# Performance work log

Measured on AMD Instinct MI355X. Metric: run time of the kernel, lower is better.

The kernel has to match this reference:

```python
import jax, jax.numpy as jnp
import numpy as np

SMOOTH = 1e-05


def setup_inputs() -> dict:
    key = jax.random.key(0)
    k1, k2 = jax.random.split(key)
    N, C, H, W = 8, 4, 1024, 1024
    inp = jax.random.normal(k1, (N, C, H, W), dtype=jnp.float32)
    target = jax.random.randint(k2, (N, H, W), 0, C, dtype=jnp.int32)
    weights = jnp.ones((C,), dtype=jnp.float32)
    return {"input": inp, "target": target, "weights": weights}


def reference(input, target, weights):
    # softmax over class dim
    p = jax.nn.softmax(input, axis=1)            # [N, C, H, W]
    C = input.shape[1]
    onehot = jax.nn.one_hot(target, C, axis=1, dtype=p.dtype)  # [N, C, H, W]
    # per-sample, per-class dice over flattened spatial dims
    inter = jnp.sum(p * onehot, axis=(2, 3))      # [N, C]
    denom = jnp.sum(p, axis=(2, 3)) + jnp.sum(onehot, axis=(2, 3))  # [N, C]
    dice = (2.0 * inter + SMOOTH) / (denom + SMOOTH)  # [N, C]
    per_class_loss = 1.0 - jnp.mean(dice, axis=0)     # [C]
    total = jnp.sum(per_class_loss * weights)
    return total
```

## Files before the change

### kernel.cpp

```cpp
#include <hip/hip_runtime.h>


#define HWPIX (1024 * 1024)
#define NCLS 4
#define NSMP 8
#define GX 256
#define TPB 256
#define NVEC (HWPIX / 4)
#define VSTRIDE (GX * TPB)
#define ITERS (NVEC / VSTRIDE)
static constexpr float SMOOTH = 1e-5f;

__global__ __launch_bounds__(TPB) void dice_partial(
    const float* __restrict__ inp,
    const int* __restrict__ tgt,
    float* __restrict__ part)
{
    const int n = blockIdx.y;
    const float4* __restrict__ in4 = (const float4*)(inp + (size_t)n * NCLS * HWPIX);
    const int4* __restrict__ tg4 = (const int4*)(tgt + (size_t)n * HWPIX);

    float psum0 = 0.f, psum1 = 0.f, psum2 = 0.f, psum3 = 0.f;
    float int0 = 0.f, int1 = 0.f, int2 = 0.f, int3 = 0.f;
    float cnt0 = 0.f, cnt1 = 0.f, cnt2 = 0.f, cnt3 = 0.f;

    const int base = blockIdx.x * TPB + threadIdx.x;

    #pragma unroll
    for (int s = 0; s < ITERS; ++s) {
        const int i = base + s * VSTRIDE;
        float4 x0 = in4[i];
        float4 x1 = in4[i + NVEC];
        float4 x2 = in4[i + 2 * NVEC];
        float4 x3 = in4[i + 3 * NVEC];
        int4 t4 = tg4[i];

        #pragma unroll
        for (int j = 0; j < 4; ++j) {
            float a = (j == 0) ? x0.x : (j == 1) ? x0.y : (j == 2) ? x0.z : x0.w;
            float b = (j == 0) ? x1.x : (j == 1) ? x1.y : (j == 2) ? x1.z : x1.w;
            float c = (j == 0) ? x2.x : (j == 1) ? x2.y : (j == 2) ? x2.z : x2.w;
            float d = (j == 0) ? x3.x : (j == 1) ? x3.y : (j == 2) ? x3.z : x3.w;
            int t   = (j == 0) ? t4.x : (j == 1) ? t4.y : (j == 2) ? t4.z : t4.w;

            float e0 = __expf(a);
            float e1 = __expf(b);
            float e2 = __expf(c);
            float e3 = __expf(d);
            float inv = __builtin_amdgcn_rcpf(e0 + e1 + e2 + e3);
            float p0 = e0 * inv, p1 = e1 * inv, p2 = e2 * inv, p3 = e3 * inv;

            psum0 += p0; psum1 += p1; psum2 += p2; psum3 += p3;
            int0 += (t == 0) ? p0 : 0.f;
            int1 += (t == 1) ? p1 : 0.f;
            int2 += (t == 2) ? p2 : 0.f;
            int3 += (t == 3) ? p3 : 0.f;
            cnt0 += (t == 0) ? 1.f : 0.f;
            cnt1 += (t == 1) ? 1.f : 0.f;
            cnt2 += (t == 2) ? 1.f : 0.f;
            cnt3 += (t == 3) ? 1.f : 0.f;
        }
    }

    float r[12] = {psum0, psum1, psum2, psum3, int0, int1, int2, int3,
                   cnt0, cnt1, cnt2, cnt3};
    #pragma unroll
    for (int off = 32; off > 0; off >>= 1) {
        #pragma unroll
        for (int k = 0; k < 12; ++k) r[k] += __shfl_down(r[k], off);
    }

    __shared__ float sred[4][12];
    const int wave = threadIdx.x >> 6;
    const int lane = threadIdx.x & 63;
    if (lane == 0) {
        #pragma unroll
        for (int k = 0; k < 12; ++k) sred[wave][k] = r[k];
    }
    __syncthreads();
    if (threadIdx.x < 12) {
        float v = sred[0][threadIdx.x] + sred[1][threadIdx.x] +
                  sred[2][threadIdx.x] + sred[3][threadIdx.x];
        part[(threadIdx.x * NSMP + n) * GX + blockIdx.x] = v;
    }
}

__global__ __launch_bounds__(1024) void dice_final(
    const float* __restrict__ part,
    const float* __restrict__ w,
    float* __restrict__ out)
{
    __shared__ float sred[96];
    const int wave = threadIdx.x >> 6;
    const int lane = threadIdx.x & 63;

    #pragma unroll
    for (int q = 0; q < 6; ++q) {
        const int s = wave * 6 + q;
        const float* seg = part + s * GX;
        float v = seg[lane] + seg[lane + 64] + seg[lane + 128] + seg[lane + 192];
        #pragma unroll
        for (int off = 32; off > 0; off >>= 1) v += __shfl_down(v, off);
        if (lane == 0) sred[s] = v;
    }
    __syncthreads();

    if (threadIdx.x == 0) {
        float total = 0.f;
        #pragma unroll
        for (int c = 0; c < NCLS; ++c) {
            float dsum = 0.f;
            #pragma unroll
            for (int n = 0; n < NSMP; ++n) {
                float psum  = sred[c * NSMP + n];
                float inter = sred[(4 + c) * NSMP + n];
                float cnt   = sred[(8 + c) * NSMP + n];
                dsum += (2.f * inter + SMOOTH) / (psum + cnt + SMOOTH);
            }
            total += w[c] * (1.f - dsum / (float)NSMP);
        }
        out[0] = total;
    }
}

extern "C" void kernel_launch(void* const* d_in, const int* in_sizes, int n_in,
                              void* d_out, int out_size, void* d_ws, size_t ws_size,
                              hipStream_t stream) {
    const float* inp = (const float*)d_in[0];
    const int* tgt   = (const int*)d_in[1];
    const float* w   = (const float*)d_in[2];
    float* out       = (float*)d_out;
    float* part      = (float*)d_ws;

    dim3 grid(GX, NSMP);
    dice_partial<<<grid, TPB, 0, stream>>>(inp, tgt, part);
    dice_final<<<1, 1024, 0, stream>>>(part, w, out);
}
```

Baseline: 39.66 us.

## Fuse final reduction into partial kernel via last-block atomic counter

Merges the two kernels into one: each block writes its partials, bumps a global atomic counter, and the last block to finish performs the final dice reduction. It also merges the prob-sum and count accumulators into one, cutting per-block partials from 12 to 8, and software-prefetches the next iteration's loads. The aim is to drop the second kernel launch and its gap, at the cost of a memset before each launch, threadfence/atomic overhead, and higher register pressure from prefetching.

```diff
diff --git a/kernel.cpp b/kernel.cpp
--- a/kernel.cpp
+++ b/kernel.cpp
@@ -9,31 +9,44 @@
 #define NVEC (HWPIX / 4)
 #define VSTRIDE (GX * TPB)
 #define ITERS (NVEC / VSTRIDE)
+#define NBLOCKS (GX * NSMP)
 static constexpr float SMOOTH = 1e-5f;
 
-__global__ __launch_bounds__(TPB) void dice_partial(
+__global__ __launch_bounds__(TPB) void dice_fused(
     const float* __restrict__ inp,
     const int* __restrict__ tgt,
-    float* __restrict__ part)
+    const float* __restrict__ w,
+    float* __restrict__ part,
+    unsigned int* __restrict__ counter,
+    float* __restrict__ out)
 {
     const int n = blockIdx.y;
     const float4* __restrict__ in4 = (const float4*)(inp + (size_t)n * NCLS * HWPIX);
     const int4* __restrict__ tg4 = (const int4*)(tgt + (size_t)n * HWPIX);
 
-    float psum0 = 0.f, psum1 = 0.f, psum2 = 0.f, psum3 = 0.f;
-    float int0 = 0.f, int1 = 0.f, int2 = 0.f, int3 = 0.f;
-    float cnt0 = 0.f, cnt1 = 0.f, cnt2 = 0.f, cnt3 = 0.f;
+    float i0 = 0.f, i1 = 0.f, i2 = 0.f, i3 = 0.f;
+    float m0 = 0.f, m1 = 0.f, m2 = 0.f, m3 = 0.f;
 
     const int base = blockIdx.x * TPB + threadIdx.x;
 
+    float4 nx0 = in4[base];
+    float4 nx1 = in4[base + NVEC];
+    float4 nx2 = in4[base + 2 * NVEC];
+    float4 nx3 = in4[base + 3 * NVEC];
+    int4 nt = tg4[base];
+
     #pragma unroll
     for (int s = 0; s < ITERS; ++s) {
-        const int i = base + s * VSTRIDE;
-        float4 x0 = in4[i];
-        float4 x1 = in4[i + NVEC];
-        float4 x2 = in4[i + 2 * NVEC];
-        float4 x3 = in4[i + 3 * NVEC];
-        int4 t4 = tg4[i];
+        float4 x0 = nx0, x1 = nx1, x2 = nx2, x3 = nx3;
+        int4 t4 = nt;
+        if (s + 1 < ITERS) {
+            const int i = base + (s + 1) * VSTRIDE;
+            nx0 = in4[i];
+            nx1 = in4[i + NVEC];
+            nx2 = in4[i + 2 * NVEC];
+            nx3 = in4[i + 3 * NVEC];
+            nt = tg4[i];
+        }
 
         #pragma unroll
         for (int j = 0; j < 4; ++j) {
@@ -50,58 +63,59 @@
             float inv = __builtin_amdgcn_rcpf(e0 + e1 + e2 + e3);
             float p0 = e0 * inv, p1 = e1 * inv, p2 = e2 * inv, p3 = e3 * inv;
 
-            psum0 += p0; psum1 += p1; psum2 += p2; psum3 += p3;
-            int0 += (t == 0) ? p0 : 0.f;
-            int1 += (t == 1) ? p1 : 0.f;
-            int2 += (t == 2) ? p2 : 0.f;
-            int3 += (t == 3) ? p3 : 0.f;
-            cnt0 += (t == 0) ? 1.f : 0.f;
-            cnt1 += (t == 1) ? 1.f : 0.f;
-            cnt2 += (t == 2) ? 1.f : 0.f;
-            cnt3 += (t == 3) ? 1.f : 0.f;
+            i0 += (t == 0) ? p0 : 0.f;
+            i1 += (t == 1) ? p1 : 0.f;
+            i2 += (t == 2) ? p2 : 0.f;
+            i3 += (t == 3) ? p3 : 0.f;
+            m0 += p0 + ((t == 0) ? 1.f : 0.f);
+            m1 += p1 + ((t == 1) ? 1.f : 0.f);
+            m2 += p2 + ((t == 2) ? 1.f : 0.f);
+            m3 += p3 + ((t == 3) ? 1.f : 0.f);
         }
     }
 
-    float r[12] = {psum0, psum1, psum2, psum3, int0, int1, int2, int3,
-                   cnt0, cnt1, cnt2, cnt3};
+    float r[8] = {i0, i1, i2, i3, m0, m1, m2, m3};
     #pragma unroll
     for (int off = 32; off > 0; off >>= 1) {
         #pragma unroll
-        for (int k = 0; k < 12; ++k) r[k] += __shfl_down(r[k], off);
+        for (int k = 0; k < 8; ++k) r[k] += __shfl_down(r[k], off);
     }
 
-    __shared__ float sred[4][12];
+    __shared__ float sred[4][8];
     const int wave = threadIdx.x >> 6;
     const int lane = threadIdx.x & 63;
     if (lane == 0) {
         #pragma unroll
-        for (int k = 0; k < 12; ++k) sred[wave][k] = r[k];
+        for (int k = 0; k < 8; ++k) sred[wave][k] = r[k];
     }
     __syncthreads();
-    if (threadIdx.x < 12) {
+    if (threadIdx.x < 8) {
         float v = sred[0][threadIdx.x] + sred[1][threadIdx.x] +
                   sred[2][threadIdx.x] + sred[3][threadIdx.x];
         part[(threadIdx.x * NSMP + n) * GX + blockIdx.x] = v;
     }
-}
 
-__global__ __launch_bounds__(1024) void dice_final(
-    const float* __restrict__ part,
-    const float* __restrict__ w,
-    float* __restrict__ out)
-{
-    __shared__ float sred[96];
-    const int wave = threadIdx.x >> 6;
-    const int lane = threadIdx.x & 63;
+    __syncthreads();
+    __shared__ bool amLast;
+    if (threadIdx.x == 0) {
+        __threadfence();
+        unsigned int old = atomicAdd(counter, 1u);
+        amLast = (old == NBLOCKS - 1);
+    }
+    __syncthreads();
+    if (!amLast) return;
 
+    __threadfence();
+
+    __shared__ float s2[64];
     #pragma unroll
-    for (int q = 0; q < 6; ++q) {
-        const int s = wave * 6 + q;
+    for (int q = 0; q < 16; ++q) {
+        const int s = wave * 16 + q;
         const float* seg = part + s * GX;
         float v = seg[lane] + seg[lane + 64] + seg[lane + 128] + seg[lane + 192];
         #pragma unroll
         for (int off = 32; off > 0; off >>= 1) v += __shfl_down(v, off);
-        if (lane == 0) sred[s] = v;
+        if (lane == 0) s2[s] = v;
     }
     __syncthreads();
 
@@ -111,11 +125,10 @@
         for (int c = 0; c < NCLS; ++c) {
             float dsum = 0.f;
             #pragma unroll
-            for (int n = 0; n < NSMP; ++n) {
-                float psum  = sred[c * NSMP + n];
-                float inter = sred[(4 + c) * NSMP + n];
-                float cnt   = sred[(8 + c) * NSMP + n];
-                dsum += (2.f * inter + SMOOTH) / (psum + cnt + SMOOTH);
+            for (int nn = 0; nn < NSMP; ++nn) {
+                float inter = s2[c * NSMP + nn];
+                float m     = s2[(4 + c) * NSMP + nn];
+                dsum += (2.f * inter + SMOOTH) / (m + SMOOTH);
             }
             total += w[c] * (1.f - dsum / (float)NSMP);
         }
@@ -131,8 +144,10 @@
     const float* w   = (const float*)d_in[2];
     float* out       = (float*)d_out;
     float* part      = (float*)d_ws;
+    unsigned int* counter = (unsigned int*)((char*)d_ws + 65536);
+
+    hipMemsetAsync(counter, 0, sizeof(unsigned int), stream);
 
     dim3 grid(GX, NSMP);
-    dice_partial<<<grid, TPB, 0, stream>>>(inp, tgt, part);
-    dice_final<<<1, 1024, 0, stream>>>(part, w, out);
+    dice_fused<<<grid, TPB, 0, stream>>>(inp, tgt, w, part, counter, out);
 }
```

After: 110.4 us. 2.78x slower.
